# Optimization experiments

Measured on AMD Instinct MI355X. Metric: run time of the kernel, lower is better.

Reference implementation:

```python
import jax, jax.numpy as jnp
import numpy as np

N = 8192
E = 262144
IN_DIM, HID_DIM, Z_DIM = 512, 256, 64


def setup_inputs() -> dict:
    key = jax.random.key(0)
    ks = jax.random.split(key, 8)
    x = jax.random.normal(ks[0], (N, IN_DIM), dtype=jnp.float32)
    edge_src = jax.random.randint(ks[1], (E,), 0, N, dtype=jnp.int32)
    edge_dst = jax.random.randint(ks[2], (E,), 0, N, dtype=jnp.int32)
    edge_w = jax.random.uniform(ks[3], (E,), dtype=jnp.float32)
    eps = jax.random.normal(ks[4], (N, Z_DIM), dtype=jnp.float32)
    # xavier-uniform linear weights (stored [in, out]); biases zero (as in torch init)
    def xavier(k, fan_in, fan_out):
        lim = float(np.sqrt(6.0 / (fan_in + fan_out)))
        return jax.random.uniform(k, (fan_in, fan_out), minval=-lim, maxval=lim, dtype=jnp.float32)
    W1 = xavier(ks[5], IN_DIM, HID_DIM)
    b1 = jnp.zeros((HID_DIM,), dtype=jnp.float32)
    Wmu = xavier(ks[6], HID_DIM, Z_DIM)
    bmu = jnp.zeros((Z_DIM,), dtype=jnp.float32)
    Wls = xavier(ks[7], HID_DIM, Z_DIM)
    bls = jnp.zeros((Z_DIM,), dtype=jnp.float32)
    return {"x": x, "edge_src": edge_src, "edge_dst": edge_dst, "edge_w": edge_w,
            "eps": eps, "W1": W1, "b1": b1, "Wmu": Wmu, "bmu": bmu, "Wls": Wls, "bls": bls}


def _spmm(edge_src, edge_dst, edge_w, h):
    # out[i] = sum_{(i,j) in edges} w_ij * h[j]  == torch.spmm(adj, h)
    return jax.ops.segment_sum(edge_w[:, None] * h[edge_dst], edge_src, num_segments=N)


def reference(x, edge_src, edge_dst, edge_w, eps, W1, b1, Wmu, bmu, Wls, bls):
    # GCN layer 1: linear -> spmm -> tanh
    h = jnp.tanh(_spmm(edge_src, edge_dst, edge_w, x @ W1 + b1))
    # mu / logstd heads (no activation)
    mu = _spmm(edge_src, edge_dst, edge_w, h @ Wmu + bmu)
    logstd = _spmm(edge_src, edge_dst, edge_w, h @ Wls + bls)
    # reparameterize (training mode): z = mu + eps * exp(logstd)
    z = mu + eps * jnp.exp(logstd)
    # inner-product decoder
    adj_logits = z @ z.T  # [N, N]
    return (z, adj_logits, mu, logstd)
```

## Files before the change

### kernel.cpp

```cpp
#include <hip/hip_runtime.h>
#include <math.h>

#define IN_DIM 512
#define HID    256
#define ZD     64

typedef short bf16x8 __attribute__((ext_vector_type(8)));
typedef float f32x4  __attribute__((ext_vector_type(4)));

__device__ inline unsigned short f2bf_rne(float f) {
    unsigned int b = __float_as_uint(f);
    b += 0x7FFFu + ((b >> 16) & 1u);
    return (unsigned short)(b >> 16);
}
__device__ inline float bf2f(unsigned short h) {
    return __uint_as_float(((unsigned int)h) << 16);
}


__global__ void k_count(const int* __restrict__ src, int* __restrict__ deg, int E) {
    int e = blockIdx.x * blockDim.x + threadIdx.x;
    if (e < E) atomicAdd(&deg[src[e]], 1);
}

__global__ __launch_bounds__(256) void k_scan(const int* __restrict__ deg,
                                              int* __restrict__ rp,
                                              int* __restrict__ nxt, int N) {
    __shared__ int sums[256];
    int t = threadIdx.x;
    int chunk = N / 256;
    int base = t * chunk;
    int run = 0;
    for (int i = 0; i < chunk; ++i) run += deg[base + i];
    sums[t] = run;
    __syncthreads();
    for (int off = 1; off < 256; off <<= 1) {
        int u = (t >= off) ? sums[t - off] : 0;
        __syncthreads();
        sums[t] += u;
        __syncthreads();
    }
    int excl = (t == 0) ? 0 : sums[t - 1];
    int run2 = excl;
    for (int i = 0; i < chunk; ++i) {
        rp[base + i]  = run2;
        nxt[base + i] = run2;
        run2 += deg[base + i];
    }
    if (t == 255) rp[N] = run2;
}

__global__ void k_scatter(const int* __restrict__ src, const int* __restrict__ dst,
                          const float* __restrict__ w, int* __restrict__ nxt,
                          int* __restrict__ col, float* __restrict__ wv, int E) {
    int e = blockIdx.x * blockDim.x + threadIdx.x;
    if (e < E) {
        int pos = atomicAdd(&nxt[src[e]], 1);
        col[pos] = dst[e];
        wv[pos]  = w[e];
    }
}

__global__ __launch_bounds__(256) void k_prep(const float* __restrict__ W1,
                                              const float* __restrict__ Wmu,
                                              const float* __restrict__ Wls,
                                              unsigned short* __restrict__ w1h,
                                              unsigned short* __restrict__ w1l,
                                              unsigned short* __restrict__ w2h,
                                              unsigned short* __restrict__ w2l,
                                              int* __restrict__ deg, int N) {
    int bid = blockIdx.x;
    int tx = threadIdx.x, ty = threadIdx.y;
    if (bid == 160) {
        int t = ty * 32 + tx;
        for (int j = t; j < N; j += 256) deg[j] = 0;
        return;
    }
    const float* src;
    unsigned short *dh, *dl;
    int Nw, ldd, rowOff, k0, n0;
    if (bid < 128) {
        src = W1; dh = w1h; dl = w1l; Nw = 256; ldd = 512; rowOff = 0;
        n0 = (bid & 7) * 32; k0 = (bid >> 3) * 32;
    } else if (bid < 144) {
        int b = bid - 128;
        src = Wmu; dh = w2h; dl = w2l; Nw = 64; ldd = 256; rowOff = 0;
        n0 = (b & 1) * 32; k0 = (b >> 1) * 32;
    } else {
        int b = bid - 144;
        src = Wls; dh = w2h; dl = w2l; Nw = 64; ldd = 256; rowOff = 64;
        n0 = (b & 1) * 32; k0 = (b >> 1) * 32;
    }
    __shared__ float tile[32][33];
    #pragma unroll
    for (int j = 0; j < 4; ++j) {
        int k = ty + j * 8;
        tile[k][tx] = src[(size_t)(k0 + k) * Nw + n0 + tx];
    }
    __syncthreads();
    #pragma unroll
    for (int j = 0; j < 4; ++j) {
        int n = ty + j * 8;
        float v = tile[tx][n];
        size_t o = (size_t)(rowOff + n0 + n) * ldd + k0 + tx;
        unsigned short hc = f2bf_rne(v);
        dh[o] = hc;
        dl[o] = f2bf_rne(v - bf2f(hc));
    }
}

__global__ __launch_bounds__(256) void k_gemm1_mfma(const float* __restrict__ x,
                                                    const unsigned short* __restrict__ wth,
                                                    const unsigned short* __restrict__ wtl,
                                                    const float* __restrict__ b1,
                                                    float* __restrict__ h0) {
    int lane = threadIdx.x & 63;
    int w    = threadIdx.x >> 6;
    int rowBase = blockIdx.y * 64 + (w >> 1) * 32;
    int colBase = blockIdx.x * 64 + (w & 1) * 32;
    int m    = lane & 15;
    int quad = lane >> 4;
    int kofs = quad * 8;

    f32x4 acc[2][2] = {};
    #pragma unroll 2
    for (int k0 = 0; k0 < IN_DIM; k0 += 32) {
        bf16x8 xhf[2], xlf[2], whf[2], wlf[2];
        #pragma unroll
        for (int g = 0; g < 2; ++g) {
            const float* px = x + (size_t)(rowBase + g * 16 + m) * IN_DIM + k0 + kofs;
            f32x4 v0 = *(const f32x4*)px;
            f32x4 v1 = *(const f32x4*)(px + 4);
            unsigned short* hp = (unsigned short*)&xhf[g];
            unsigned short* lp = (unsigned short*)&xlf[g];
            #pragma unroll
            for (int j = 0; j < 4; ++j) {
                unsigned short hc0 = f2bf_rne(v0[j]);
                hp[j] = hc0;
                lp[j] = f2bf_rne(v0[j] - bf2f(hc0));
                unsigned short hc1 = f2bf_rne(v1[j]);
                hp[4 + j] = hc1;
                lp[4 + j] = f2bf_rne(v1[j] - bf2f(hc1));
            }
            size_t woff = (size_t)(colBase + g * 16 + m) * IN_DIM + k0 + kofs;
            whf[g] = *(const bf16x8*)&wth[woff];
            wlf[g] = *(const bf16x8*)&wtl[woff];
        }
        #pragma unroll
        for (int xg = 0; xg < 2; ++xg)
            #pragma unroll
            for (int wg = 0; wg < 2; ++wg) {
                acc[xg][wg] = __builtin_amdgcn_mfma_f32_16x16x32_bf16(whf[wg], xhf[xg], acc[xg][wg], 0, 0, 0);
                acc[xg][wg] = __builtin_amdgcn_mfma_f32_16x16x32_bf16(whf[wg], xlf[xg], acc[xg][wg], 0, 0, 0);
                acc[xg][wg] = __builtin_amdgcn_mfma_f32_16x16x32_bf16(wlf[wg], xhf[xg], acc[xg][wg], 0, 0, 0);
            }
    }
    #pragma unroll
    for (int wg = 0; wg < 2; ++wg) {
        float4 bv = *(const float4*)&b1[colBase + wg * 16 + quad * 4];
        float bb[4] = {bv.x, bv.y, bv.z, bv.w};
        #pragma unroll
        for (int xg = 0; xg < 2; ++xg) {
            f32x4 o = acc[xg][wg];
            #pragma unroll
            for (int r = 0; r < 4; ++r) o[r] += bb[r];
            *(f32x4*)&h0[(size_t)(rowBase + xg * 16 + m) * HID + colBase + wg * 16 + quad * 4] = o;
        }
    }
}

__global__ __launch_bounds__(256) void k_spmm_tanh(const int* __restrict__ rp,
                                                   const int* __restrict__ col,
                                                   const float* __restrict__ wv,
                                                   const float* __restrict__ h0,
                                                   float* __restrict__ h) {
    __shared__ int scol[256];
    __shared__ float sw[256];
    int i = blockIdx.x, t = threadIdx.x;
    int s = rp[i], e = rp[i + 1];
    float acc = 0.f;
    for (int cs = s; cs < e; cs += 256) {
        int n = min(256, e - cs);
        __syncthreads();
        if (t < n) { scol[t] = col[cs + t]; sw[t] = wv[cs + t]; }
        __syncthreads();
        #pragma unroll 4
        for (int p = 0; p < n; ++p)
            acc += sw[p] * h0[(size_t)scol[p] * HID + t];
    }
    h[(size_t)i * HID + t] = tanhf(acc);
}

__global__ __launch_bounds__(256) void k_heads_mfma(const float* __restrict__ h,
                                                    const unsigned short* __restrict__ w2h,
                                                    const unsigned short* __restrict__ w2l,
                                                    const float* __restrict__ bmu,
                                                    const float* __restrict__ bls,
                                                    float* __restrict__ hh) {
    int lane = threadIdx.x & 63;
    int w    = threadIdx.x >> 6;
    int rowBase = blockIdx.y * 64 + (w >> 1) * 32;
    int colBase = blockIdx.x * 64 + (w & 1) * 32;
    int m    = lane & 15;
    int quad = lane >> 4;
    int kofs = quad * 8;

    f32x4 acc[2][2] = {};
    #pragma unroll 2
    for (int k0 = 0; k0 < HID; k0 += 32) {
        bf16x8 xhf[2], xlf[2], whf[2], wlf[2];
        #pragma unroll
        for (int g = 0; g < 2; ++g) {
            const float* ph = h + (size_t)(rowBase + g * 16 + m) * HID + k0 + kofs;
            f32x4 v0 = *(const f32x4*)ph;
            f32x4 v1 = *(const f32x4*)(ph + 4);
            unsigned short* hp = (unsigned short*)&xhf[g];
            unsigned short* lp = (unsigned short*)&xlf[g];
            #pragma unroll
            for (int j = 0; j < 4; ++j) {
                unsigned short hc0 = f2bf_rne(v0[j]);
                hp[j] = hc0;
                lp[j] = f2bf_rne(v0[j] - bf2f(hc0));
                unsigned short hc1 = f2bf_rne(v1[j]);
                hp[4 + j] = hc1;
                lp[4 + j] = f2bf_rne(v1[j] - bf2f(hc1));
            }
            size_t woff = (size_t)(colBase + g * 16 + m) * HID + k0 + kofs;
            whf[g] = *(const bf16x8*)&w2h[woff];
            wlf[g] = *(const bf16x8*)&w2l[woff];
        }
        #pragma unroll
        for (int xg = 0; xg < 2; ++xg)
            #pragma unroll
            for (int wg = 0; wg < 2; ++wg) {
                acc[xg][wg] = __builtin_amdgcn_mfma_f32_16x16x32_bf16(whf[wg], xhf[xg], acc[xg][wg], 0, 0, 0);
                acc[xg][wg] = __builtin_amdgcn_mfma_f32_16x16x32_bf16(whf[wg], xlf[xg], acc[xg][wg], 0, 0, 0);
                acc[xg][wg] = __builtin_amdgcn_mfma_f32_16x16x32_bf16(wlf[wg], xhf[xg], acc[xg][wg], 0, 0, 0);
            }
    }
    #pragma unroll
    for (int wg = 0; wg < 2; ++wg) {
        int cg = colBase + wg * 16 + quad * 4;
        float4 bv = (cg < 64) ? *(const float4*)&bmu[cg] : *(const float4*)&bls[cg - 64];
        float bb[4] = {bv.x, bv.y, bv.z, bv.w};
        #pragma unroll
        for (int xg = 0; xg < 2; ++xg) {
            f32x4 o = acc[xg][wg];
            #pragma unroll
            for (int r = 0; r < 4; ++r) o[r] += bb[r];
            *(f32x4*)&hh[(size_t)(rowBase + xg * 16 + m) * 128 + cg] = o;
        }
    }
}

__global__ __launch_bounds__(128) void k_spmm_heads(const int* __restrict__ rp,
                                                    const int* __restrict__ col,
                                                    const float* __restrict__ wv,
                                                    const float* __restrict__ hh,
                                                    const float* __restrict__ eps,
                                                    float* __restrict__ mu,
                                                    float* __restrict__ ls,
                                                    float* __restrict__ z,
                                                    unsigned short* __restrict__ zb) {
    __shared__ int scol[128];
    __shared__ float sw[128];
    __shared__ float sls[64];
    int i = blockIdx.x, t = threadIdx.x;
    int s = rp[i], e = rp[i + 1];
    float acc = 0.f;
    for (int cs = s; cs < e; cs += 128) {
        int n = min(128, e - cs);
        __syncthreads();
        if (t < n) { scol[t] = col[cs + t]; sw[t] = wv[cs + t]; }
        __syncthreads();
        #pragma unroll 4
        for (int p = 0; p < n; ++p)
            acc += sw[p] * hh[(size_t)scol[p] * 128 + t];
    }
    if (t >= 64) { ls[(size_t)i * ZD + t - 64] = acc; sls[t - 64] = acc; }
    __syncthreads();
    if (t < 64) {
        size_t o = (size_t)i * ZD + t;
        mu[o] = acc;
        float zz = acc + eps[o] * expf(sls[t]);
        z[o] = zz;
        zb[o] = f2bf_rne(zz);
    }
}

__global__ __launch_bounds__(256) void k_zzt_mfma(const unsigned short* __restrict__ zb,
                                                  float* __restrict__ out, int N) {
    int lane = threadIdx.x & 63;
    int w    = threadIdx.x >> 6;
    int waveRow = blockIdx.y * 128 + (w >> 1) * 64;
    int waveCol = blockIdx.x * 128 + (w & 1) * 64;
    int m    = lane & 15;
    int quad = lane >> 4;
    int kofs = quad * 8;

    bf16x8 a[4][2], b[4][2];
    #pragma unroll
    for (int rg = 0; rg < 4; ++rg) {
        const unsigned short* pr = zb + (size_t)(waveRow + rg * 16 + m) * ZD + kofs;
        const unsigned short* pc = zb + (size_t)(waveCol + rg * 16 + m) * ZD + kofs;
        a[rg][0] = *(const bf16x8*)pr;
        a[rg][1] = *(const bf16x8*)(pr + 32);
        b[rg][0] = *(const bf16x8*)pc;
        b[rg][1] = *(const bf16x8*)(pc + 32);
    }

    f32x4 acc[4][4] = {};
    #pragma unroll
    for (int rg = 0; rg < 4; ++rg)
        #pragma unroll
        for (int cg = 0; cg < 4; ++cg) {
            acc[rg][cg] = __builtin_amdgcn_mfma_f32_16x16x32_bf16(b[cg][0], a[rg][0], acc[rg][cg], 0, 0, 0);
            acc[rg][cg] = __builtin_amdgcn_mfma_f32_16x16x32_bf16(b[cg][1], a[rg][1], acc[rg][cg], 0, 0, 0);
        }

    #pragma unroll
    for (int rg = 0; rg < 4; ++rg) {
        size_t rowOff = (size_t)(waveRow + rg * 16 + m) * N;
        #pragma unroll
        for (int cg = 0; cg < 4; ++cg) {
            f32x4* po = (f32x4*)&out[rowOff + waveCol + cg * 16 + quad * 4];
            __builtin_nontemporal_store(acc[rg][cg], po);
        }
    }
}


extern "C" void kernel_launch(void* const* d_in, const int* in_sizes, int n_in,
                              void* d_out, int out_size, void* d_ws, size_t ws_size,
                              hipStream_t stream) {
    const float* x    = (const float*)d_in[0];
    const int*   esrc = (const int*)d_in[1];
    const int*   edst = (const int*)d_in[2];
    const float* ew   = (const float*)d_in[3];
    const float* eps  = (const float*)d_in[4];
    const float* W1   = (const float*)d_in[5];
    const float* b1   = (const float*)d_in[6];
    const float* Wmu  = (const float*)d_in[7];
    const float* bmu  = (const float*)d_in[8];
    const float* Wls  = (const float*)d_in[9];
    const float* bls  = (const float*)d_in[10];
    int N = in_sizes[0] / IN_DIM;
    int E = in_sizes[1];

    char* base = (char*)d_ws;
    size_t o = 0;
    #define ALLOC(ptr, type, count) type* ptr = (type*)(base + o); o = (o + (size_t)(count) * sizeof(type) + 63) & ~(size_t)63;
    ALLOC(h0,  float, (size_t)N * HID)
    ALLOC(h,   float, (size_t)N * HID)
    ALLOC(hh,  float, (size_t)N * 128)
    ALLOC(rp,  int,   N + 1)
    ALLOC(deg, int,   N)
    ALLOC(nxt, int,   N)
    ALLOC(col, int,   E)
    ALLOC(wv,  float, E)
    ALLOC(zb,  unsigned short, (size_t)N * ZD)
    ALLOC(w1h, unsigned short, (size_t)IN_DIM * HID)
    ALLOC(w1l, unsigned short, (size_t)IN_DIM * HID)
    ALLOC(w2h, unsigned short, (size_t)128 * HID)
    ALLOC(w2l, unsigned short, (size_t)128 * HID)
    #undef ALLOC

    float* out_z   = (float*)d_out;
    float* out_adj = out_z + (size_t)N * ZD;
    float* out_mu  = out_adj + (size_t)N * N;
    float* out_ls  = out_mu + (size_t)N * ZD;

    k_prep<<<161, dim3(32, 8), 0, stream>>>(W1, Wmu, Wls, w1h, w1l, w2h, w2l, deg, N);

    k_count<<<(E + 255) / 256, 256, 0, stream>>>(esrc, deg, E);
    k_scan<<<1, 256, 0, stream>>>(deg, rp, nxt, N);
    k_scatter<<<(E + 255) / 256, 256, 0, stream>>>(esrc, edst, ew, nxt, col, wv, E);

    k_gemm1_mfma<<<dim3(HID / 64, N / 64), 256, 0, stream>>>(x, w1h, w1l, b1, h0);

    k_spmm_tanh<<<N, 256, 0, stream>>>(rp, col, wv, h0, h);

    k_heads_mfma<<<dim3(2, N / 64), 256, 0, stream>>>(h, w2h, w2l, bmu, bls, hh);

    k_spmm_heads<<<N, 128, 0, stream>>>(rp, col, wv, hh, eps, out_mu, out_ls, out_z, zb);

    dim3 g2(N / 128, N / 128);
    k_zzt_mfma<<<g2, 256, 0, stream>>>(zb, out_adj, N);
}
```

Before: 462.8 us.

## Switch intermediate GEMMs and activations from split-bf16 to single fp16

Replaces the three-pass split-bf16 MFMA emulation in both dense GEMMs with a single fp16 MFMA, and stores the intermediate activations h0, h and hh as fp16 instead of fp32. This cuts MFMA work roughly threefold, removes the hi/lo split arithmetic, and halves the bytes gathered in both SpMM passes. The scan kernel is also widened to 1024 threads. The cost is reduced precision in the intermediates, since fp16 has less mantissa than the emulated near-fp32 path, and fp16 range limits could matter.

```diff
diff --git a/kernel.cpp b/kernel.cpp
--- a/kernel.cpp
+++ b/kernel.cpp
@@ -7,15 +7,15 @@
 
 typedef short bf16x8 __attribute__((ext_vector_type(8)));
 typedef float f32x4  __attribute__((ext_vector_type(4)));
+typedef _Float16 f16;
+typedef _Float16 f16x8 __attribute__((ext_vector_type(8)));
+typedef _Float16 f16x4 __attribute__((ext_vector_type(4)));
 
 __device__ inline unsigned short f2bf_rne(float f) {
     unsigned int b = __float_as_uint(f);
     b += 0x7FFFu + ((b >> 16) & 1u);
     return (unsigned short)(b >> 16);
 }
-__device__ inline float bf2f(unsigned short h) {
-    return __uint_as_float(((unsigned int)h) << 16);
-}
 
 
 __global__ void k_count(const int* __restrict__ src, int* __restrict__ deg, int E) {
@@ -23,18 +23,18 @@
     if (e < E) atomicAdd(&deg[src[e]], 1);
 }
 
-__global__ __launch_bounds__(256) void k_scan(const int* __restrict__ deg,
-                                              int* __restrict__ rp,
-                                              int* __restrict__ nxt, int N) {
-    __shared__ int sums[256];
+__global__ __launch_bounds__(1024) void k_scan(const int* __restrict__ deg,
+                                               int* __restrict__ rp,
+                                               int* __restrict__ nxt, int N) {
+    __shared__ int sums[1024];
     int t = threadIdx.x;
-    int chunk = N / 256;
+    int chunk = N / 1024;
     int base = t * chunk;
     int run = 0;
     for (int i = 0; i < chunk; ++i) run += deg[base + i];
     sums[t] = run;
     __syncthreads();
-    for (int off = 1; off < 256; off <<= 1) {
+    for (int off = 1; off < 1024; off <<= 1) {
         int u = (t >= off) ? sums[t - off] : 0;
         __syncthreads();
         sums[t] += u;
@@ -47,7 +47,7 @@
         nxt[base + i] = run2;
         run2 += deg[base + i];
     }
-    if (t == 255) rp[N] = run2;
+    if (t == 1023) rp[N] = run2;
 }
 
 __global__ void k_scatter(const int* __restrict__ src, const int* __restrict__ dst,
@@ -64,10 +64,8 @@
 __global__ __launch_bounds__(256) void k_prep(const float* __restrict__ W1,
                                               const float* __restrict__ Wmu,
                                               const float* __restrict__ Wls,
-                                              unsigned short* __restrict__ w1h,
-                                              unsigned short* __restrict__ w1l,
-                                              unsigned short* __restrict__ w2h,
-                                              unsigned short* __restrict__ w2l,
+                                              f16* __restrict__ w1t,
+                                              f16* __restrict__ w2t,
                                               int* __restrict__ deg, int N) {
     int bid = blockIdx.x;
     int tx = threadIdx.x, ty = threadIdx.y;
@@ -77,18 +75,18 @@
         return;
     }
     const float* src;
-    unsigned short *dh, *dl;
+    f16* dst;
     int Nw, ldd, rowOff, k0, n0;
     if (bid < 128) {
-        src = W1; dh = w1h; dl = w1l; Nw = 256; ldd = 512; rowOff = 0;
+        src = W1; dst = w1t; Nw = 256; ldd = 512; rowOff = 0;
         n0 = (bid & 7) * 32; k0 = (bid >> 3) * 32;
     } else if (bid < 144) {
         int b = bid - 128;
-        src = Wmu; dh = w2h; dl = w2l; Nw = 64; ldd = 256; rowOff = 0;
+        src = Wmu; dst = w2t; Nw = 64; ldd = 256; rowOff = 0;
         n0 = (b & 1) * 32; k0 = (b >> 1) * 32;
     } else {
         int b = bid - 144;
-        src = Wls; dh = w2h; dl = w2l; Nw = 64; ldd = 256; rowOff = 64;
+        src = Wls; dst = w2t; Nw = 64; ldd = 256; rowOff = 64;
         n0 = (b & 1) * 32; k0 = (b >> 1) * 32;
     }
     __shared__ float tile[32][33];
@@ -101,19 +99,14 @@
     #pragma unroll
     for (int j = 0; j < 4; ++j) {
         int n = ty + j * 8;
-        float v = tile[tx][n];
-        size_t o = (size_t)(rowOff + n0 + n) * ldd + k0 + tx;
-        unsigned short hc = f2bf_rne(v);
-        dh[o] = hc;
-        dl[o] = f2bf_rne(v - bf2f(hc));
+        dst[(size_t)(rowOff + n0 + n) * ldd + k0 + tx] = (f16)tile[tx][n];
     }
 }
 
 __global__ __launch_bounds__(256) void k_gemm1_mfma(const float* __restrict__ x,
-                                                    const unsigned short* __restrict__ wth,
-                                                    const unsigned short* __restrict__ wtl,
+                                                    const f16* __restrict__ w1t,
                                                     const float* __restrict__ b1,
-                                                    float* __restrict__ h0) {
+                                                    f16* __restrict__ h0) {
     int lane = threadIdx.x & 63;
     int w    = threadIdx.x >> 6;
     int rowBase = blockIdx.y * 64 + (w >> 1) * 32;
@@ -123,37 +116,25 @@
     int kofs = quad * 8;
 
     f32x4 acc[2][2] = {};
-    #pragma unroll 2
+    #pragma unroll 4
     for (int k0 = 0; k0 < IN_DIM; k0 += 32) {
-        bf16x8 xhf[2], xlf[2], whf[2], wlf[2];
+        f16x8 xf[2], wf[2];
         #pragma unroll
         for (int g = 0; g < 2; ++g) {
             const float* px = x + (size_t)(rowBase + g * 16 + m) * IN_DIM + k0 + kofs;
             f32x4 v0 = *(const f32x4*)px;
             f32x4 v1 = *(const f32x4*)(px + 4);
-            unsigned short* hp = (unsigned short*)&xhf[g];
-            unsigned short* lp = (unsigned short*)&xlf[g];
-            #pragma unroll
-            for (int j = 0; j < 4; ++j) {
-                unsigned short hc0 = f2bf_rne(v0[j]);
-                hp[j] = hc0;
-                lp[j] = f2bf_rne(v0[j] - bf2f(hc0));
-                unsigned short hc1 = f2bf_rne(v1[j]);
-                hp[4 + j] = hc1;
-                lp[4 + j] = f2bf_rne(v1[j] - bf2f(hc1));
-            }
-            size_t woff = (size_t)(colBase + g * 16 + m) * IN_DIM + k0 + kofs;
-            whf[g] = *(const bf16x8*)&wth[woff];
-            wlf[g] = *(const bf16x8*)&wtl[woff];
+            f16x8 xv;
+            #pragma unroll
+            for (int j = 0; j < 4; ++j) { xv[j] = (f16)v0[j]; xv[4 + j] = (f16)v1[j]; }
+            xf[g] = xv;
+            wf[g] = *(const f16x8*)&w1t[(size_t)(colBase + g * 16 + m) * IN_DIM + k0 + kofs];
         }
         #pragma unroll
         for (int xg = 0; xg < 2; ++xg)
             #pragma unroll
-            for (int wg = 0; wg < 2; ++wg) {
-                acc[xg][wg] = __builtin_amdgcn_mfma_f32_16x16x32_bf16(whf[wg], xhf[xg], acc[xg][wg], 0, 0, 0);
-                acc[xg][wg] = __builtin_amdgcn_mfma_f32_16x16x32_bf16(whf[wg], xlf[xg], acc[xg][wg], 0, 0, 0);
-                acc[xg][wg] = __builtin_amdgcn_mfma_f32_16x16x32_bf16(wlf[wg], xhf[xg], acc[xg][wg], 0, 0, 0);
-            }
+            for (int wg = 0; wg < 2; ++wg)
+                acc[xg][wg] = __builtin_amdgcn_mfma_f32_16x16x32_f16(wf[wg], xf[xg], acc[xg][wg], 0, 0, 0);
     }
     #pragma unroll
     for (int wg = 0; wg < 2; ++wg) {
@@ -161,10 +142,10 @@
         float bb[4] = {bv.x, bv.y, bv.z, bv.w};
         #pragma unroll
         for (int xg = 0; xg < 2; ++xg) {
-            f32x4 o = acc[xg][wg];
-            #pragma unroll
-            for (int r = 0; r < 4; ++r) o[r] += bb[r];
-            *(f32x4*)&h0[(size_t)(rowBase + xg * 16 + m) * HID + colBase + wg * 16 + quad * 4] = o;
+            f16x4 o;
+            #pragma unroll
+            for (int r = 0; r < 4; ++r) o[r] = (f16)(acc[xg][wg][r] + bb[r]);
+            *(f16x4*)&h0[(size_t)(rowBase + xg * 16 + m) * HID + colBase + wg * 16 + quad * 4] = o;
         }
     }
 }
@@ -172,8 +153,8 @@
 __global__ __launch_bounds__(256) void k_spmm_tanh(const int* __restrict__ rp,
                                                    const int* __restrict__ col,
                                                    const float* __restrict__ wv,
-                                                   const float* __restrict__ h0,
-                                                   float* __restrict__ h) {
+                                                   const f16* __restrict__ h0,
+                                                   f16* __restrict__ h) {
     __shared__ int scol[256];
     __shared__ float sw[256];
     int i = blockIdx.x, t = threadIdx.x;
@@ -186,17 +167,16 @@
         __syncthreads();
         #pragma unroll 4
         for (int p = 0; p < n; ++p)
-            acc += sw[p] * h0[(size_t)scol[p] * HID + t];
-    }
-    h[(size_t)i * HID + t] = tanhf(acc);
-}
-
-__global__ __launch_bounds__(256) void k_heads_mfma(const float* __restrict__ h,
-                                                    const unsigned short* __restrict__ w2h,
-                                                    const unsigned short* __restrict__ w2l,
+            acc += sw[p] * (float)h0[(size_t)scol[p] * HID + t];
+    }
+    h[(size_t)i * HID + t] = (f16)tanhf(acc);
+}
+
+__global__ __launch_bounds__(256) void k_heads_mfma(const f16* __restrict__ h,
+                                                    const f16* __restrict__ w2t,
                                                     const float* __restrict__ bmu,
                                                     const float* __restrict__ bls,
-                                                    float* __restrict__ hh) {
+                                                    f16* __restrict__ hh) {
     int lane = threadIdx.x & 63;
     int w    = threadIdx.x >> 6;
     int rowBase = blockIdx.y * 64 + (w >> 1) * 32;
@@ -206,37 +186,19 @@
     int kofs = quad * 8;
 
     f32x4 acc[2][2] = {};
-    #pragma unroll 2
+    #pragma unroll 4
     for (int k0 = 0; k0 < HID; k0 += 32) {
-        bf16x8 xhf[2], xlf[2], whf[2], wlf[2];
+        f16x8 hf[2], wf[2];
         #pragma unroll
         for (int g = 0; g < 2; ++g) {
-            const float* ph = h + (size_t)(rowBase + g * 16 + m) * HID + k0 + kofs;
-            f32x4 v0 = *(const f32x4*)ph;
-            f32x4 v1 = *(const f32x4*)(ph + 4);
-            unsigned short* hp = (unsigned short*)&xhf[g];
-            unsigned short* lp = (unsigned short*)&xlf[g];
-            #pragma unroll
-            for (int j = 0; j < 4; ++j) {
-                unsigned short hc0 = f2bf_rne(v0[j]);
-                hp[j] = hc0;
-                lp[j] = f2bf_rne(v0[j] - bf2f(hc0));
-                unsigned short hc1 = f2bf_rne(v1[j]);
-                hp[4 + j] = hc1;
-                lp[4 + j] = f2bf_rne(v1[j] - bf2f(hc1));
-            }
-            size_t woff = (size_t)(colBase + g * 16 + m) * HID + k0 + kofs;
-            whf[g] = *(const bf16x8*)&w2h[woff];
-            wlf[g] = *(const bf16x8*)&w2l[woff];
+            hf[g] = *(const f16x8*)&h[(size_t)(rowBase + g * 16 + m) * HID + k0 + kofs];
+            wf[g] = *(const f16x8*)&w2t[(size_t)(colBase + g * 16 + m) * HID + k0 + kofs];
         }
         #pragma unroll
         for (int xg = 0; xg < 2; ++xg)
             #pragma unroll
-            for (int wg = 0; wg < 2; ++wg) {
-                acc[xg][wg] = __builtin_amdgcn_mfma_f32_16x16x32_bf16(whf[wg], xhf[xg], acc[xg][wg], 0, 0, 0);
-                acc[xg][wg] = __builtin_amdgcn_mfma_f32_16x16x32_bf16(whf[wg], xlf[xg], acc[xg][wg], 0, 0, 0);
-                acc[xg][wg] = __builtin_amdgcn_mfma_f32_16x16x32_bf16(wlf[wg], xhf[xg], acc[xg][wg], 0, 0, 0);
-            }
+            for (int wg = 0; wg < 2; ++wg)
+                acc[xg][wg] = __builtin_amdgcn_mfma_f32_16x16x32_f16(wf[wg], hf[xg], acc[xg][wg], 0, 0, 0);
     }
     #pragma unroll
     for (int wg = 0; wg < 2; ++wg) {
@@ -245,10 +207,10 @@
         float bb[4] = {bv.x, bv.y, bv.z, bv.w};
         #pragma unroll
         for (int xg = 0; xg < 2; ++xg) {
-            f32x4 o = acc[xg][wg];
-            #pragma unroll
-            for (int r = 0; r < 4; ++r) o[r] += bb[r];
-            *(f32x4*)&hh[(size_t)(rowBase + xg * 16 + m) * 128 + cg] = o;
+            f16x4 o;
+            #pragma unroll
+            for (int r = 0; r < 4; ++r) o[r] = (f16)(acc[xg][wg][r] + bb[r]);
+            *(f16x4*)&hh[(size_t)(rowBase + xg * 16 + m) * 128 + cg] = o;
         }
     }
 }
@@ -256,7 +218,7 @@
 __global__ __launch_bounds__(128) void k_spmm_heads(const int* __restrict__ rp,
                                                     const int* __restrict__ col,
                                                     const float* __restrict__ wv,
-                                                    const float* __restrict__ hh,
+                                                    const f16* __restrict__ hh,
                                                     const float* __restrict__ eps,
                                                     float* __restrict__ mu,
                                                     float* __restrict__ ls,
@@ -275,7 +237,7 @@
         __syncthreads();
         #pragma unroll 4
         for (int p = 0; p < n; ++p)
-            acc += sw[p] * hh[(size_t)scol[p] * 128 + t];
+            acc += sw[p] * (float)hh[(size_t)scol[p] * 128 + t];
     }
     if (t >= 64) { ls[(size_t)i * ZD + t - 64] = acc; sls[t - 64] = acc; }
     __syncthreads();
@@ -350,19 +312,17 @@
     char* base = (char*)d_ws;
     size_t o = 0;
     #define ALLOC(ptr, type, count) type* ptr = (type*)(base + o); o = (o + (size_t)(count) * sizeof(type) + 63) & ~(size_t)63;
-    ALLOC(h0,  float, (size_t)N * HID)
-    ALLOC(h,   float, (size_t)N * HID)
-    ALLOC(hh,  float, (size_t)N * 128)
+    ALLOC(h0,  f16,   (size_t)N * HID)
+    ALLOC(h,   f16,   (size_t)N * HID)
+    ALLOC(hh,  f16,   (size_t)N * 128)
     ALLOC(rp,  int,   N + 1)
     ALLOC(deg, int,   N)
     ALLOC(nxt, int,   N)
     ALLOC(col, int,   E)
     ALLOC(wv,  float, E)
     ALLOC(zb,  unsigned short, (size_t)N * ZD)
-    ALLOC(w1h, unsigned short, (size_t)IN_DIM * HID)
-    ALLOC(w1l, unsigned short, (size_t)IN_DIM * HID)
-    ALLOC(w2h, unsigned short, (size_t)128 * HID)
-    ALLOC(w2l, unsigned short, (size_t)128 * HID)
+    ALLOC(w1t, f16,   (size_t)HID * IN_DIM)
+    ALLOC(w2t, f16,   (size_t)128 * HID)
     #undef ALLOC
 
     float* out_z   = (float*)d_out;
@@ -370,17 +330,17 @@
     float* out_mu  = out_adj + (size_t)N * N;
     float* out_ls  = out_mu + (size_t)N * ZD;
 
-    k_prep<<<161, dim3(32, 8), 0, stream>>>(W1, Wmu, Wls, w1h, w1l, w2h, w2l, deg, N);
+    k_prep<<<161, dim3(32, 8), 0, stream>>>(W1, Wmu, Wls, w1t, w2t, deg, N);
 
     k_count<<<(E + 255) / 256, 256, 0, stream>>>(esrc, deg, E);
-    k_scan<<<1, 256, 0, stream>>>(deg, rp, nxt, N);
+    k_scan<<<1, 1024, 0, stream>>>(deg, rp, nxt, N);
     k_scatter<<<(E + 255) / 256, 256, 0, stream>>>(esrc, edst, ew, nxt, col, wv, E);
 
-    k_gemm1_mfma<<<dim3(HID / 64, N / 64), 256, 0, stream>>>(x, w1h, w1l, b1, h0);
+    k_gemm1_mfma<<<dim3(HID / 64, N / 64), 256, 0, stream>>>(x, w1t, b1, h0);
 
     k_spmm_tanh<<<N, 256, 0, stream>>>(rp, col, wv, h0, h);
 
-    k_heads_mfma<<<dim3(2, N / 64), 256, 0, stream>>>(h, w2h, w2l, bmu, bls, hh);
+    k_heads_mfma<<<dim3(2, N / 64), 256, 0, stream>>>(h, w2t, bmu, bls, hh);
 
     k_spmm_heads<<<N, 128, 0, stream>>>(rp, col, wv, hh, eps, out_mu, out_ls, out_z, zb);
 
```

New measurement: 429.8 us. -7.1%, faster.
